# Optimization experiments

Measured on AMD Instinct MI355X. Metric: run time of the kernel, lower is better.

## Reference

```python
import jax, jax.numpy as jnp
import numpy as np

B, N, F = 2, 2048, 256
H = 8
O = F // H  # nhid = 32
L = 3       # stacked GraphAttentionLayers
ALPHA = 0.2
NEG = jnp.float32(-1e15)


def setup_inputs() -> dict:
    key = jax.random.key(0)
    ks = jax.random.split(key, 6)
    x = jax.random.normal(ks[0], (B, N, F), dtype=jnp.float32)
    adj = jax.random.randint(ks[1], (B, N, N), 0, 2, dtype=jnp.int32)
    # per-layer multi-head params: W [L,H,F,O], a [L,H,2O]
    W_heads = jax.random.normal(ks[2], (L, H, F, O), dtype=jnp.float32) * 0.1
    a_heads = jax.random.normal(ks[3], (L, H, 2 * O), dtype=jnp.float32) * 0.1
    # per-layer out_att params (single head, F->F)
    W_out = jax.random.normal(ks[4], (L, F, F), dtype=jnp.float32) * 0.05
    a_out = jax.random.normal(ks[5], (L, 2 * F), dtype=jnp.float32) * 0.05
    return {"x": x, "adj": adj, "W_heads": W_heads, "a_heads": a_heads,
            "W_out": W_out, "a_out": a_out}


def _gat_heads(h, mask, W, a1, a2):
    """h: [B,N,F], mask: [B,N,N] bool, W: [H,F,O], a1/a2: [H,O] -> [B,H,N,O]."""
    Wh = jnp.einsum('bnf,hfo->bhno', h, W)
    s1 = jnp.einsum('bhno,ho->bhn', Wh, a1)   # a[:O] projection
    s2 = jnp.einsum('bhno,ho->bhn', Wh, a2)   # a[O:] projection
    e = s1[:, :, :, None] + s2[:, :, None, :]  # additive score [B,H,N,N]
    e = jnp.where(e > 0, e, ALPHA * e)         # LeakyReLU(alpha)
    e = jnp.where(mask[:, None, :, :], e, NEG)
    att = jax.nn.softmax(e, axis=-1)           # dropout is identity in eval
    hp = jnp.einsum('bhnm,bhmo->bhno', att, Wh)
    return jax.nn.elu(hp)                      # activate_function inside head


def reference(x, adj, W_heads, a_heads, W_out, a_out):
    mask = adj > 0
    h = x
    for l in range(L):
        a1 = a_heads[l, :, :O]
        a2 = a_heads[l, :, O:]
        hh = _gat_heads(h, mask, W_heads[l], a1, a2)      # [B,H,N,O]
        h = jnp.transpose(hh, (0, 2, 1, 3)).reshape(B, N, F)  # concat heads
        ao1 = a_out[l, :F][None]
        ao2 = a_out[l, F:][None]
        ho = _gat_heads(h, mask, W_out[l][None], ao1, ao2)[:, 0]  # [B,N,F]
        h = jax.nn.elu(ho)  # extra F.elu in GraphAttentionLayer (elu twice)
    return h
```

## Files before the change

### kernel.cpp

```cpp
#include <hip/hip_runtime.h>
#include <math.h>

#if __has_builtin(__builtin_amdgcn_exp2f)
#define EXP2(x) __builtin_amdgcn_exp2f(x)
#else
#define EXP2(x) exp2f(x)
#endif

#define ALPHA_LRELU 0.2f
#define LOG2E 1.4426950408889634f
#define ESHIFT 6.0f
#define BIGM 1024.0f

constexpr int Bc = 2, Nn = 2048, Ff = 256, Hh = 8, Oo = 32;

typedef _Float16 f16;
typedef f16 f16x8 __attribute__((ext_vector_type(8)));
typedef f16 f16x4 __attribute__((ext_vector_type(4)));
typedef float f32x4 __attribute__((ext_vector_type(4)));
typedef unsigned long long u64;
typedef unsigned u32;

__global__ __launch_bounds__(256) void prep_kernel(
    const int* __restrict__ adj, const float* __restrict__ x,
    const float* __restrict__ W_heads, const float* __restrict__ W_out,
    u32* __restrict__ maskT, f16* __restrict__ Af, f16* __restrict__ WTF,
    float* __restrict__ sbuf) {
    const int B = blockIdx.x;
    const int t = threadIdx.x;
    int g = B * 256 + t;
    if (g < 221184) sbuf[g] = 0.f;

    if (B < 768) {
        for (int idx = g; idx < Bc * Nn * Nn; idx += 768 * 256) {
            u64 bl = __ballot(adj[idx] != 0);
            int lane = t & 63;
            int i = (idx >> 11) & 2047;
            int b = idx >> 22;
            int c32 = ((idx & 2047) & ~63) >> 5;
            if (lane == 0)
                maskT[((size_t)b * 64 + c32) * 2048 + i] = (u32)bl;
            else if (lane == 1)
                maskT[((size_t)b * 64 + c32 + 1) * 2048 + i] = (u32)(bl >> 32);
        }
    } else if (B < 896) {
        int w = t >> 6, lane = t & 63;
        int am = lane & 15, aq = lane >> 4;
#pragma unroll
        for (int it = 0; it < 4; ++it) {
            int slot = (B - 768) * 4 + w + it * 512;
            int mt = slot >> 3, c = slot & 7;
            const float* ap = x + ((size_t)mt * 16 + am) * Ff + c * 32 + aq * 8;
            f32x4 v0 = *(const f32x4*)ap;
            f32x4 v1 = *(const f32x4*)(ap + 4);
            f16x8 o;
#pragma unroll
            for (int i = 0; i < 4; ++i) { o[i] = (f16)v0[i]; o[4 + i] = (f16)v1[i]; }
            *(f16x8*)&Af[(size_t)slot * 512 + lane * 8] = o;
        }
    } else {
#pragma unroll
        for (int it = 0; it < 3; ++it) {
            int unit = (B - 896) * 3 + it;
            int y = unit >> 6, bx = unit & 63;
            int ll = y >> 1, st = y & 1;
            int col = bx * 4 + (t >> 6);
            int k0 = (t & 63) * 4;
            const float* src;
            int stride;
            if (st == 0) {
                src = W_heads + (((size_t)ll * Hh + (col >> 5)) * Ff) * Oo + (col & 31);
                stride = Oo;
            } else {
                src = W_out + (size_t)ll * Ff * Ff + col;
                stride = Ff;
            }
            f16x4 v;
#pragma unroll
            for (int i = 0; i < 4; ++i) v[i] = (f16)src[(size_t)(k0 + i) * stride];
            int cg = col >> 4, am = col & 15;
            int c = k0 >> 5, aq = (k0 >> 3) & 3, i0 = k0 & 7;
            *(f16x4*)&WTF[(((size_t)y * 16 + cg) * 8 + c) * 512 +
                          (aq * 16 + am) * 8 + i0] = v;
        }
    }
}

__global__ __launch_bounds__(256) void gemm_wave(
    const f16* __restrict__ Af, const f16* __restrict__ WTF,
    const float* __restrict__ pa, f16* __restrict__ WhFrag,
    float* __restrict__ s1, float* __restrict__ s2,
    int G, int Ofull, int oshift) {
    int t = threadIdx.x;
    int w = t >> 6, lane = t & 63;
    int am = lane & 15, aq = lane >> 4;
    int mt = blockIdx.x * 4 + w;
    int colb = blockIdx.y * 32;

    const f16* ap = Af + (size_t)(mt * 8) * 512 + lane * 8;
    const f16* bp0 = WTF + (size_t)((colb >> 4) * 8) * 512 + lane * 8;
    const f16* bp1 = bp0 + 8 * 512;

    f16x8 av[8], bv0[8], bv1[8];
#pragma unroll
    for (int c = 0; c < 8; ++c) {
        av[c] = *(const f16x8*)(ap + c * 512);
        bv0[c] = *(const f16x8*)(bp0 + c * 512);
        bv1[c] = *(const f16x8*)(bp1 + c * 512);
    }
    f32x4 acc0 = {0.f, 0.f, 0.f, 0.f}, acc1 = acc0;
#pragma unroll
    for (int c = 0; c < 8; ++c) {
        acc0 = __builtin_amdgcn_mfma_f32_16x16x32_f16(av[c], bv0[c], acc0, 0, 0, 0);
        acc1 = __builtin_amdgcn_mfma_f32_16x16x32_f16(av[c], bv1[c], acc1, 0, 0, 0);
    }

    int m0 = mt * 16;
    int b = m0 >> 11;
    int nn0 = (m0 & 2047) + aq * 4;
    int cO = (m0 & 2047) >> 5;
    int aq_p = ((mt & 1) << 1) | (aq >> 1);
    int i0p = (aq & 1) << 2;
    int g = colb >> oshift;
    size_t bg = (size_t)b * G + g;
    int cg = (colb & (Ofull - 1)) >> 4;

    f16x4 c40, c41;
#pragma unroll
    for (int e = 0; e < 4; ++e) { c40[e] = (f16)acc0[e]; c41[e] = (f16)acc1[e]; }
    *(f16x4*)&WhFrag[(((bg * (Ofull >> 4) + cg) * 64 + cO) * 512) +
                     (aq_p * 16 + am) * 8 + i0p] = c40;
    *(f16x4*)&WhFrag[(((bg * (Ofull >> 4) + cg + 1) * 64 + cO) * 512) +
                     (aq_p * 16 + am) * 8 + i0p] = c41;

    int o0 = (colb & (Ofull - 1)) + am;
    const float* a1p = pa + 2 * (size_t)g * Ofull;
    float a10 = a1p[o0], a11 = a1p[o0 + 16];
    float a20 = a1p[Ofull + o0], a21 = a1p[Ofull + o0 + 16];
#pragma unroll
    for (int e = 0; e < 4; ++e) {
        float p1 = acc0[e] * a10 + acc1[e] * a11;
        float p2 = acc0[e] * a20 + acc1[e] * a21;
#pragma unroll
        for (int s = 1; s < 16; s <<= 1) {
            p1 += __shfl_xor(p1, s);
            p2 += __shfl_xor(p2, s);
        }
        if (am == 0) {
            size_t sidx = bg * Nn + nn0 + e;
            atomicAdd(&s1[sidx], p1);
            atomicAdd(&s2[sidx], p2);
        }
    }
}

template <int CGW, int NW, bool OUT, bool FINAL>
__global__ __launch_bounds__(NW * 64) void attn_kernel(
    const f16* __restrict__ WhFrag, const float* __restrict__ s1,
    const float* __restrict__ s2, const u32* __restrict__ maskT,
    float* __restrict__ dst, f16* __restrict__ AfOut) {
    constexpr float C0 = -ESHIFT * LOG2E - BIGM;
    constexpr int NCG = OUT ? 16 : 2;
    constexpr int COLS = (NW / 4) * CGW * 16;
    constexpr int TSTR = COLS + 8;
    __shared__ float Ls[NW][2][64];
    __shared__ float As[NW][64][2 * CGW * 4];
    __shared__ f16 T[2][16 * TSTR];

    int t = threadIdx.x;
    int w = t >> 6, lane = t & 63;
    int am = lane & 15, aq = lane >> 4;
    int ch = w >> 2;
    int js = w & 3;
    int i0 = blockIdx.x * 32;
    int bz = blockIdx.z;
    int b = OUT ? bz : (bz >> 3);
    int cg0 = OUT ? blockIdx.y * ((NW / 4) * CGW) + ch * CGW : 0;
    int dstcol = OUT ? cg0 * 16 : (bz & 7) * Oo;

    const f16* bp[CGW];
#pragma unroll
    for (int i = 0; i < CGW; ++i)
        bp[i] = WhFrag + ((size_t)bz * NCG + cg0 + i) * 64 * 512 + lane * 8;
    const float* s2p = s2 + (size_t)bz * Nn + aq * 8;
    float s1v0 = s1[(size_t)bz * Nn + i0 + am];
    float s1v1 = s1[(size_t)bz * Nn + i0 + 16 + am];
    const u32* mtp0 = maskT + (size_t)b * 64 * 2048 + i0 + am;
    const u32* mtp1 = mtp0 + 16;

    f32x4 acc[2][CGW] = {};
    float lacc0 = 0.f, lacc1 = 0.f;

    int cbeg = js * 16, cend = cbeg + 16;

    f16x8 xb[CGW], yb[CGW];
    f32x4 xv0, xv1, yv0, yv1;
    u32 xm0, xm1, ym0, ym1;
    auto ld = [&](int c, f16x8 (&bb)[CGW], f32x4& v0, f32x4& v1,
                  u32& m0, u32& m1) {
#pragma unroll
        for (int i = 0; i < CGW; ++i) bb[i] = *(const f16x8*)(bp[i] + c * 512);
        v0 = *(const f32x4*)(s2p + c * 32);
        v1 = *(const f32x4*)(s2p + c * 32 + 4);
        m0 = mtp0[c * 2048];
        m1 = mtp1[c * 2048];
    };
    auto comp = [&](f16x8 (&bb)[CGW], f32x4 v0, f32x4 v1, u32 m0, u32 m1) {
        u32 bits0 = (m0 >> (aq * 8)) & 0xffu;
        u32 bits1 = (m1 >> (aq * 8)) & 0xffu;
        f16x8 af0, af1;
#pragma unroll
        for (int k = 0; k < 8; ++k) {
            float sv = (k < 4 ? v0[k] : v1[k - 4]);
            float x0 = s1v0 + sv;
            float x1 = s1v1 + sv;
            float lr0 = fmaxf(x0, ALPHA_LRELU * x0);
            float lr1 = fmaxf(x1, ALPHA_LRELU * x1);
            float bf0 = (float)((bits0 >> k) & 1u);
            float bf1 = (float)((bits1 >> k) & 1u);
            float p0 = EXP2(fmaf(bf0, BIGM, fmaf(lr0, LOG2E, C0)));
            float p1 = EXP2(fmaf(bf1, BIGM, fmaf(lr1, LOG2E, C0)));
            lacc0 += p0;
            lacc1 += p1;
            af0[k] = (f16)p0;
            af1[k] = (f16)p1;
        }
#pragma unroll
        for (int i = 0; i < CGW; ++i) {
            acc[0][i] = __builtin_amdgcn_mfma_f32_16x16x32_f16(af0, bb[i], acc[0][i], 0, 0, 0);
            acc[1][i] = __builtin_amdgcn_mfma_f32_16x16x32_f16(af1, bb[i], acc[1][i], 0, 0, 0);
        }
    };

    ld(cbeg, xb, xv0, xv1, xm0, xm1);
    ld(cbeg + 1, yb, yv0, yv1, ym0, ym1);
    for (int c = cbeg; c < cend; c += 2) {
        comp(xb, xv0, xv1, xm0, xm1);
        ld(c + 2 < cend ? c + 2 : cbeg, xb, xv0, xv1, xm0, xm1);
        comp(yb, yv0, yv1, ym0, ym1);
        ld(c + 3 < cend ? c + 3 : cbeg, yb, yv0, yv1, ym0, ym1);
    }

    lacc0 += __shfl_xor(lacc0, 16);
    lacc0 += __shfl_xor(lacc0, 32);
    lacc1 += __shfl_xor(lacc1, 16);
    lacc1 += __shfl_xor(lacc1, 32);

    Ls[w][0][lane] = lacc0;
    Ls[w][1][lane] = lacc1;
#pragma unroll
    for (int tt = 0; tt < 2; ++tt)
#pragma unroll
        for (int i = 0; i < CGW; ++i)
#pragma unroll
            for (int e = 0; e < 4; ++e)
                As[w][lane][tt * CGW * 4 + i * 4 + e] = acc[tt][i][e];
    __syncthreads();

    if ((w & 3) < 2) {
        int tt = w & 3;
        float lt = Ls[ch * 4 + 0][tt][lane] + Ls[ch * 4 + 1][tt][lane] +
                   Ls[ch * 4 + 2][tt][lane] + Ls[ch * 4 + 3][tt][lane];
        f16* Tw = T[tt];
#pragma unroll
        for (int i = 0; i < CGW; ++i) {
            f32x4 a;
#pragma unroll
            for (int e = 0; e < 4; ++e)
                a[e] = As[ch * 4 + 0][lane][tt * CGW * 4 + i * 4 + e] +
                       As[ch * 4 + 1][lane][tt * CGW * 4 + i * 4 + e] +
                       As[ch * 4 + 2][lane][tt * CGW * 4 + i * 4 + e] +
                       As[ch * 4 + 3][lane][tt * CGW * 4 + i * 4 + e];
#pragma unroll
            for (int e = 0; e < 4; ++e) {
                int r = aq * 4 + e;
                float li = __shfl(lt, r);
                float v = a[e] / li;
                v = v > 0.f ? v : __expf(v) - 1.f;
                if (OUT) v = v > 0.f ? v : __expf(v) - 1.f;
                if (FINAL) {
                    dst[((size_t)b * Nn + i0 + tt * 16 + r) * Ff + dstcol +
                        i * 16 + am] = v;
                } else {
                    Tw[r * TSTR + ch * CGW * 16 + i * 16 + am] = (f16)v;
                }
            }
        }
        if (!FINAL) {
            int mt = (b * Nn + i0 + tt * 16) >> 4;
#pragma unroll
            for (int s = 0; s < CGW / 2; ++s) {
                f16x8 o = *(const f16x8*)&Tw[am * TSTR + ch * CGW * 16 +
                                             s * 32 + aq * 8];
                int c = (dstcol >> 5) + s;
                *(f16x8*)&AfOut[(size_t)(mt * 8 + c) * 512 + lane * 8] = o;
            }
        }
    }
}

extern "C" void kernel_launch(void* const* d_in, const int* in_sizes, int n_in,
                              void* d_out, int out_size, void* d_ws, size_t ws_size,
                              hipStream_t stream) {
    const float* x = (const float*)d_in[0];
    const int* adj = (const int*)d_in[1];
    const float* W_heads = (const float*)d_in[2];
    const float* a_heads = (const float*)d_in[3];
    const float* W_out = (const float*)d_in[4];
    const float* a_out = (const float*)d_in[5];
    float* out = (float*)d_out;

    float* ws = (float*)d_ws;
    const size_t M = (size_t)Bc * Nn * Ff;
    f16* Af_a = (f16*)ws;
    f16* Af_b = (f16*)(ws + M / 2);
    f16* WhFrag = (f16*)(ws + M);
    u32* maskT = (u32*)(ws + 3 * M / 2);
    f16* WTF = (f16*)(ws + 3 * M / 2 + M / 4);
    float* sbuf = ws + 3 * M / 2 + M / 4 + 196608;
    const size_t SH = (size_t)Bc * Hh * Nn;
    const size_t SO = (size_t)Bc * Nn;
    const size_t SL = 2 * SH + 2 * SO;

    prep_kernel<<<1024, 256, 0, stream>>>(adj, x, W_heads, W_out,
                                          maskT, Af_a, WTF, sbuf);

    for (int l = 0; l < 3; ++l) {
        float* s1h = sbuf + l * SL;
        float* s2h = s1h + SH;
        float* s1o = s2h + SH;
        float* s2o = s1o + SO;

        gemm_wave<<<dim3((Bc * Nn) / 64, Ff / 32), 256, 0, stream>>>(
            Af_a, WTF + (size_t)(2 * l) * Ff * Ff,
            a_heads + (size_t)l * Hh * 2 * Oo, WhFrag, s1h, s2h, Hh, Oo, 5);
        attn_kernel<2, 4, false, false><<<dim3(Nn / 32, 1, Bc * Hh), 256, 0, stream>>>(
            WhFrag, s1h, s2h, maskT, nullptr, Af_b);

        gemm_wave<<<dim3((Bc * Nn) / 64, Ff / 32), 256, 0, stream>>>(
            Af_b, WTF + (size_t)(2 * l + 1) * Ff * Ff,
            a_out + (size_t)l * 2 * Ff, WhFrag, s1o, s2o, 1, Ff, 8);
        if (l == 2) {
            attn_kernel<4, 8, true, true><<<dim3(Nn / 32, Ff / 128, Bc), 512, 0, stream>>>(
                WhFrag, s1o, s2o, maskT, out, nullptr);
        } else {
            attn_kernel<4, 8, true, false><<<dim3(Nn / 32, Ff / 128, Bc), 512, 0, stream>>>(
                WhFrag, s1o, s2o, maskT, nullptr, Af_a);
        }
    }
}
```

Baseline: 265.3 us.

## Fuse all layers into a persistent megakernel with hierarchical grid barriers

Replaces the prep kernel and the 12 per-layer GEMM and attention launches with one persistent kernel of 512 blocks. The blocks step through the prep, GEMM and attention phases and meet at a two-level atomic grid barrier between phases. A small init kernel zeroes the score accumulators and the barrier counters. This removes per-launch overhead and the tail idle time at each kernel boundary. In exchange, the OUT attention phase now runs on 256-thread blocks instead of 512, and the barrier assumes all 512 blocks are resident at once, which hangs if they are not.

```diff
diff --git a/kernel.cpp b/kernel.cpp
--- a/kernel.cpp
+++ b/kernel.cpp
@@ -13,6 +13,7 @@
 #define BIGM 1024.0f
 
 constexpr int Bc = 2, Nn = 2048, Ff = 256, Hh = 8, Oo = 32;
+constexpr int NBLK = 512;
 
 typedef _Float16 f16;
 typedef f16 f16x8 __attribute__((ext_vector_type(8)));
@@ -21,18 +22,259 @@
 typedef unsigned long long u64;
 typedef unsigned u32;
 
-__global__ __launch_bounds__(256) void prep_kernel(
+__global__ __launch_bounds__(256) void init_kernel(float* __restrict__ sbuf,
+                                                   u32* __restrict__ bar) {
+    for (int g = blockIdx.x * 256 + threadIdx.x; g < 221184; g += NBLK * 256)
+        sbuf[g] = 0.f;
+    int g = blockIdx.x * 256 + threadIdx.x;
+    if (g < 544) bar[g] = 0;
+}
+
+__device__ __forceinline__ void gridbar(u32* bar, int ph) {
+    __syncthreads();
+    if (threadIdx.x == 0) {
+        __threadfence();
+        u32* lv1 = bar + 32 + (blockIdx.x & 15) * 32;
+        u32 old = __hip_atomic_fetch_add(lv1, 1u, __ATOMIC_RELAXED,
+                                         __HIP_MEMORY_SCOPE_AGENT);
+        if (old == (u32)(ph * 32 + 31))
+            __hip_atomic_fetch_add(bar, 1u, __ATOMIC_RELAXED,
+                                   __HIP_MEMORY_SCOPE_AGENT);
+        while (__hip_atomic_load(bar, __ATOMIC_RELAXED,
+                                 __HIP_MEMORY_SCOPE_AGENT) <
+               (u32)(ph * 16 + 16))
+            __builtin_amdgcn_s_sleep(2);
+        __threadfence();
+    }
+    __syncthreads();
+}
+
+__device__ __forceinline__ void gemm_phase(
+    const f16* __restrict__ Af, const f16* __restrict__ WTF,
+    const float* __restrict__ pa, f16* __restrict__ WhFrag,
+    float* __restrict__ s1, float* __restrict__ s2,
+    int G, int Ofull, int oshift, int xb, int yb) {
+    int t = threadIdx.x;
+    int w = t >> 6, lane = t & 63;
+    int am = lane & 15, aq = lane >> 4;
+    int mt = xb * 4 + w;
+    int colb = yb * 32;
+
+    const f16* ap = Af + (size_t)(mt * 8) * 512 + lane * 8;
+    const f16* bp0 = WTF + (size_t)((colb >> 4) * 8) * 512 + lane * 8;
+    const f16* bp1 = bp0 + 8 * 512;
+
+    f16x8 av[8], bv0[8], bv1[8];
+#pragma unroll
+    for (int c = 0; c < 8; ++c) {
+        av[c] = *(const f16x8*)(ap + c * 512);
+        bv0[c] = *(const f16x8*)(bp0 + c * 512);
+        bv1[c] = *(const f16x8*)(bp1 + c * 512);
+    }
+    f32x4 acc0 = {0.f, 0.f, 0.f, 0.f}, acc1 = acc0;
+#pragma unroll
+    for (int c = 0; c < 8; ++c) {
+        acc0 = __builtin_amdgcn_mfma_f32_16x16x32_f16(av[c], bv0[c], acc0, 0, 0, 0);
+        acc1 = __builtin_amdgcn_mfma_f32_16x16x32_f16(av[c], bv1[c], acc1, 0, 0, 0);
+    }
+
+    int m0 = mt * 16;
+    int b = m0 >> 11;
+    int nn0 = (m0 & 2047) + aq * 4;
+    int cO = (m0 & 2047) >> 5;
+    int aq_p = ((mt & 1) << 1) | (aq >> 1);
+    int i0p = (aq & 1) << 2;
+    int g = colb >> oshift;
+    size_t bg = (size_t)b * G + g;
+    int cg = (colb & (Ofull - 1)) >> 4;
+
+    f16x4 c40, c41;
+#pragma unroll
+    for (int e = 0; e < 4; ++e) { c40[e] = (f16)acc0[e]; c41[e] = (f16)acc1[e]; }
+    *(f16x4*)&WhFrag[(((bg * (Ofull >> 4) + cg) * 64 + cO) * 512) +
+                     (aq_p * 16 + am) * 8 + i0p] = c40;
+    *(f16x4*)&WhFrag[(((bg * (Ofull >> 4) + cg + 1) * 64 + cO) * 512) +
+                     (aq_p * 16 + am) * 8 + i0p] = c41;
+
+    int o0 = (colb & (Ofull - 1)) + am;
+    const float* a1p = pa + 2 * (size_t)g * Ofull;
+    float a10 = a1p[o0], a11 = a1p[o0 + 16];
+    float a20 = a1p[Ofull + o0], a21 = a1p[Ofull + o0 + 16];
+#pragma unroll
+    for (int e = 0; e < 4; ++e) {
+        float p1 = acc0[e] * a10 + acc1[e] * a11;
+        float p2 = acc0[e] * a20 + acc1[e] * a21;
+#pragma unroll
+        for (int s = 1; s < 16; s <<= 1) {
+            p1 += __shfl_xor(p1, s);
+            p2 += __shfl_xor(p2, s);
+        }
+        if (am == 0) {
+            size_t sidx = bg * Nn + nn0 + e;
+            atomicAdd(&s1[sidx], p1);
+            atomicAdd(&s2[sidx], p2);
+        }
+    }
+}
+
+template <int CGW, bool OUT, bool FINAL>
+__device__ __forceinline__ void attn_phase(
+    const f16* __restrict__ WhFrag, const float* __restrict__ s1,
+    const float* __restrict__ s2, const u32* __restrict__ maskT,
+    float* __restrict__ dst, f16* __restrict__ AfOut,
+    int xb, int yq, int bz,
+    float* __restrict__ LsS, float* __restrict__ AsS, f16* __restrict__ TS) {
+    constexpr float C0 = -ESHIFT * LOG2E - BIGM;
+    constexpr int NCG = OUT ? 16 : 2;
+    constexpr int TSTR = 72;
+
+    int t = threadIdx.x;
+    int w = t >> 6, lane = t & 63;
+    int am = lane & 15, aq = lane >> 4;
+    int i0 = xb * 32;
+    int b = OUT ? bz : (bz >> 3);
+    int cg0 = OUT ? yq * CGW : 0;
+    int dstcol = OUT ? cg0 * 16 : (bz & 7) * Oo;
+
+    const f16* bp[CGW];
+#pragma unroll
+    for (int i = 0; i < CGW; ++i)
+        bp[i] = WhFrag + ((size_t)bz * NCG + cg0 + i) * 64 * 512 + lane * 8;
+    const float* s2p = s2 + (size_t)bz * Nn + aq * 8;
+    float s1v0 = s1[(size_t)bz * Nn + i0 + am];
+    float s1v1 = s1[(size_t)bz * Nn + i0 + 16 + am];
+    const u32* mtp0 = maskT + (size_t)b * 64 * 2048 + i0 + am;
+    const u32* mtp1 = mtp0 + 16;
+
+    f32x4 acc[2][CGW] = {};
+    float lacc0 = 0.f, lacc1 = 0.f;
+
+    int cbeg = w * 16, cend = cbeg + 16;
+
+    f16x8 xb_[CGW], yb_[CGW];
+    f32x4 xv0, xv1, yv0, yv1;
+    u32 xm0, xm1, ym0, ym1;
+    auto ld = [&](int c, f16x8 (&bb)[CGW], f32x4& v0, f32x4& v1,
+                  u32& m0, u32& m1) {
+#pragma unroll
+        for (int i = 0; i < CGW; ++i) bb[i] = *(const f16x8*)(bp[i] + c * 512);
+        v0 = *(const f32x4*)(s2p + c * 32);
+        v1 = *(const f32x4*)(s2p + c * 32 + 4);
+        m0 = mtp0[c * 2048];
+        m1 = mtp1[c * 2048];
+    };
+    auto comp = [&](f16x8 (&bb)[CGW], f32x4 v0, f32x4 v1, u32 m0, u32 m1) {
+        u32 bits0 = (m0 >> (aq * 8)) & 0xffu;
+        u32 bits1 = (m1 >> (aq * 8)) & 0xffu;
+        f16x8 af0, af1;
+#pragma unroll
+        for (int k = 0; k < 8; ++k) {
+            float sv = (k < 4 ? v0[k] : v1[k - 4]);
+            float x0 = s1v0 + sv;
+            float x1 = s1v1 + sv;
+            float lr0 = fmaxf(x0, ALPHA_LRELU * x0);
+            float lr1 = fmaxf(x1, ALPHA_LRELU * x1);
+            float bf0 = (float)((bits0 >> k) & 1u);
+            float bf1 = (float)((bits1 >> k) & 1u);
+            float p0 = EXP2(fmaf(bf0, BIGM, fmaf(lr0, LOG2E, C0)));
+            float p1 = EXP2(fmaf(bf1, BIGM, fmaf(lr1, LOG2E, C0)));
+            lacc0 += p0;
+            lacc1 += p1;
+            af0[k] = (f16)p0;
+            af1[k] = (f16)p1;
+        }
+#pragma unroll
+        for (int i = 0; i < CGW; ++i) {
+            acc[0][i] = __builtin_amdgcn_mfma_f32_16x16x32_f16(af0, bb[i], acc[0][i], 0, 0, 0);
+            acc[1][i] = __builtin_amdgcn_mfma_f32_16x16x32_f16(af1, bb[i], acc[1][i], 0, 0, 0);
+        }
+    };
+
+    ld(cbeg, xb_, xv0, xv1, xm0, xm1);
+    ld(cbeg + 1, yb_, yv0, yv1, ym0, ym1);
+    for (int c = cbeg; c < cend; c += 2) {
+        comp(xb_, xv0, xv1, xm0, xm1);
+        ld(c + 2 < cend ? c + 2 : cbeg, xb_, xv0, xv1, xm0, xm1);
+        comp(yb_, yv0, yv1, ym0, ym1);
+        ld(c + 3 < cend ? c + 3 : cbeg, yb_, yv0, yv1, ym0, ym1);
+    }
+
+    lacc0 += __shfl_xor(lacc0, 16);
+    lacc0 += __shfl_xor(lacc0, 32);
+    lacc1 += __shfl_xor(lacc1, 16);
+    lacc1 += __shfl_xor(lacc1, 32);
+
+    LsS[(w * 2 + 0) * 64 + lane] = lacc0;
+    LsS[(w * 2 + 1) * 64 + lane] = lacc1;
+#pragma unroll
+    for (int tt = 0; tt < 2; ++tt)
+#pragma unroll
+        for (int i = 0; i < CGW; ++i)
+#pragma unroll
+            for (int e = 0; e < 4; ++e)
+                AsS[(w * 64 + lane) * 32 + tt * CGW * 4 + i * 4 + e] =
+                    acc[tt][i][e];
+    __syncthreads();
+
+    if (w < 2) {
+        int tt = w;
+        float lt = LsS[(0 * 2 + tt) * 64 + lane] + LsS[(1 * 2 + tt) * 64 + lane] +
+                   LsS[(2 * 2 + tt) * 64 + lane] + LsS[(3 * 2 + tt) * 64 + lane];
+        f16* Tw = &TS[tt * 16 * TSTR];
+#pragma unroll
+        for (int i = 0; i < CGW; ++i) {
+            f32x4 a;
+#pragma unroll
+            for (int e = 0; e < 4; ++e)
+                a[e] = AsS[(0 * 64 + lane) * 32 + tt * CGW * 4 + i * 4 + e] +
+                       AsS[(1 * 64 + lane) * 32 + tt * CGW * 4 + i * 4 + e] +
+                       AsS[(2 * 64 + lane) * 32 + tt * CGW * 4 + i * 4 + e] +
+                       AsS[(3 * 64 + lane) * 32 + tt * CGW * 4 + i * 4 + e];
+#pragma unroll
+            for (int e = 0; e < 4; ++e) {
+                int r = aq * 4 + e;
+                float li = __shfl(lt, r);
+                float v = a[e] / li;
+                v = v > 0.f ? v : __expf(v) - 1.f;
+                if (OUT) v = v > 0.f ? v : __expf(v) - 1.f;
+                if (FINAL) {
+                    dst[((size_t)b * Nn + i0 + tt * 16 + r) * Ff + dstcol +
+                        i * 16 + am] = v;
+                } else {
+                    Tw[r * TSTR + i * 16 + am] = (f16)v;
+                }
+            }
+        }
+        if (!FINAL) {
+            int mt = (b * Nn + i0 + tt * 16) >> 4;
+#pragma unroll
+            for (int s = 0; s < CGW / 2; ++s) {
+                f16x8 o = *(const f16x8*)&Tw[am * TSTR + s * 32 + aq * 8];
+                int c = (dstcol >> 5) + s;
+                *(f16x8*)&AfOut[(size_t)(mt * 8 + c) * 512 + lane * 8] = o;
+            }
+        }
+    }
+    __syncthreads();
+}
+
+__global__ __launch_bounds__(256, 2) void mega_kernel(
     const int* __restrict__ adj, const float* __restrict__ x,
-    const float* __restrict__ W_heads, const float* __restrict__ W_out,
-    u32* __restrict__ maskT, f16* __restrict__ Af, f16* __restrict__ WTF,
-    float* __restrict__ sbuf) {
+    const float* __restrict__ W_heads, const float* __restrict__ a_heads,
+    const float* __restrict__ W_out, const float* __restrict__ a_out,
+    float* __restrict__ out, f16* __restrict__ Af_a, f16* __restrict__ Af_b,
+    f16* __restrict__ WhFrag, u32* __restrict__ maskT, f16* __restrict__ WTF,
+    float* __restrict__ sbuf, u32* __restrict__ bar) {
+    __shared__ float LsS[4 * 2 * 64];
+    __shared__ float AsS[4 * 64 * 32];
+    __shared__ f16 TS[2 * 16 * 72];
+
     const int B = blockIdx.x;
     const int t = threadIdx.x;
-    int g = B * 256 + t;
-    if (g < 221184) sbuf[g] = 0.f;
-
-    if (B < 768) {
-        for (int idx = g; idx < Bc * Nn * Nn; idx += 768 * 256) {
+    int ph = 0;
+
+    if (B < 384) {
+        for (int idx = B * 256 + t; idx < Bc * Nn * Nn; idx += 384 * 256) {
             u64 bl = __ballot(adj[idx] != 0);
             int lane = t & 63;
             int i = (idx >> 11) & 2047;
@@ -43,12 +285,12 @@
             else if (lane == 1)
                 maskT[((size_t)b * 64 + c32 + 1) * 2048 + i] = (u32)(bl >> 32);
         }
-    } else if (B < 896) {
+    } else if (B < 448) {
         int w = t >> 6, lane = t & 63;
         int am = lane & 15, aq = lane >> 4;
 #pragma unroll
-        for (int it = 0; it < 4; ++it) {
-            int slot = (B - 768) * 4 + w + it * 512;
+        for (int it = 0; it < 8; ++it) {
+            int slot = (B - 384) * 4 + w + it * 256;
             int mt = slot >> 3, c = slot & 7;
             const float* ap = x + ((size_t)mt * 16 + am) * Ff + c * 32 + aq * 8;
             f32x4 v0 = *(const f32x4*)ap;
@@ -56,12 +298,12 @@
             f16x8 o;
 #pragma unroll
             for (int i = 0; i < 4; ++i) { o[i] = (f16)v0[i]; o[4 + i] = (f16)v1[i]; }
-            *(f16x8*)&Af[(size_t)slot * 512 + lane * 8] = o;
+            *(f16x8*)&Af_a[(size_t)slot * 512 + lane * 8] = o;
         }
     } else {
 #pragma unroll
-        for (int it = 0; it < 3; ++it) {
-            int unit = (B - 896) * 3 + it;
+        for (int it = 0; it < 6; ++it) {
+            int unit = (B - 448) * 6 + it;
             int y = unit >> 6, bx = unit & 63;
             int ll = y >> 1, st = y & 1;
             int col = bx * 4 + (t >> 6);
@@ -84,217 +326,38 @@
                           (aq * 16 + am) * 8 + i0] = v;
         }
     }
-}
-
-__global__ __launch_bounds__(256) void gemm_wave(
-    const f16* __restrict__ Af, const f16* __restrict__ WTF,
-    const float* __restrict__ pa, f16* __restrict__ WhFrag,
-    float* __restrict__ s1, float* __restrict__ s2,
-    int G, int Ofull, int oshift) {
-    int t = threadIdx.x;
-    int w = t >> 6, lane = t & 63;
-    int am = lane & 15, aq = lane >> 4;
-    int mt = blockIdx.x * 4 + w;
-    int colb = blockIdx.y * 32;
-
-    const f16* ap = Af + (size_t)(mt * 8) * 512 + lane * 8;
-    const f16* bp0 = WTF + (size_t)((colb >> 4) * 8) * 512 + lane * 8;
-    const f16* bp1 = bp0 + 8 * 512;
-
-    f16x8 av[8], bv0[8], bv1[8];
-#pragma unroll
-    for (int c = 0; c < 8; ++c) {
-        av[c] = *(const f16x8*)(ap + c * 512);
-        bv0[c] = *(const f16x8*)(bp0 + c * 512);
-        bv1[c] = *(const f16x8*)(bp1 + c * 512);
-    }
-    f32x4 acc0 = {0.f, 0.f, 0.f, 0.f}, acc1 = acc0;
-#pragma unroll
-    for (int c = 0; c < 8; ++c) {
-        acc0 = __builtin_amdgcn_mfma_f32_16x16x32_f16(av[c], bv0[c], acc0, 0, 0, 0);
-        acc1 = __builtin_amdgcn_mfma_f32_16x16x32_f16(av[c], bv1[c], acc1, 0, 0, 0);
-    }
-
-    int m0 = mt * 16;
-    int b = m0 >> 11;
-    int nn0 = (m0 & 2047) + aq * 4;
-    int cO = (m0 & 2047) >> 5;
-    int aq_p = ((mt & 1) << 1) | (aq >> 1);
-    int i0p = (aq & 1) << 2;
-    int g = colb >> oshift;
-    size_t bg = (size_t)b * G + g;
-    int cg = (colb & (Ofull - 1)) >> 4;
-
-    f16x4 c40, c41;
-#pragma unroll
-    for (int e = 0; e < 4; ++e) { c40[e] = (f16)acc0[e]; c41[e] = (f16)acc1[e]; }
-    *(f16x4*)&WhFrag[(((bg * (Ofull >> 4) + cg) * 64 + cO) * 512) +
-                     (aq_p * 16 + am) * 8 + i0p] = c40;
-    *(f16x4*)&WhFrag[(((bg * (Ofull >> 4) + cg + 1) * 64 + cO) * 512) +
-                     (aq_p * 16 + am) * 8 + i0p] = c41;
-
-    int o0 = (colb & (Ofull - 1)) + am;
-    const float* a1p = pa + 2 * (size_t)g * Ofull;
-    float a10 = a1p[o0], a11 = a1p[o0 + 16];
-    float a20 = a1p[Ofull + o0], a21 = a1p[Ofull + o0 + 16];
-#pragma unroll
-    for (int e = 0; e < 4; ++e) {
-        float p1 = acc0[e] * a10 + acc1[e] * a11;
-        float p2 = acc0[e] * a20 + acc1[e] * a21;
-#pragma unroll
-        for (int s = 1; s < 16; s <<= 1) {
-            p1 += __shfl_xor(p1, s);
-            p2 += __shfl_xor(p2, s);
-        }
-        if (am == 0) {
-            size_t sidx = bg * Nn + nn0 + e;
-            atomicAdd(&s1[sidx], p1);
-            atomicAdd(&s2[sidx], p2);
-        }
-    }
-}
-
-template <int CGW, int NW, bool OUT, bool FINAL>
-__global__ __launch_bounds__(NW * 64) void attn_kernel(
-    const f16* __restrict__ WhFrag, const float* __restrict__ s1,
-    const float* __restrict__ s2, const u32* __restrict__ maskT,
-    float* __restrict__ dst, f16* __restrict__ AfOut) {
-    constexpr float C0 = -ESHIFT * LOG2E - BIGM;
-    constexpr int NCG = OUT ? 16 : 2;
-    constexpr int COLS = (NW / 4) * CGW * 16;
-    constexpr int TSTR = COLS + 8;
-    __shared__ float Ls[NW][2][64];
-    __shared__ float As[NW][64][2 * CGW * 4];
-    __shared__ f16 T[2][16 * TSTR];
-
-    int t = threadIdx.x;
-    int w = t >> 6, lane = t & 63;
-    int am = lane & 15, aq = lane >> 4;
-    int ch = w >> 2;
-    int js = w & 3;
-    int i0 = blockIdx.x * 32;
-    int bz = blockIdx.z;
-    int b = OUT ? bz : (bz >> 3);
-    int cg0 = OUT ? blockIdx.y * ((NW / 4) * CGW) + ch * CGW : 0;
-    int dstcol = OUT ? cg0 * 16 : (bz & 7) * Oo;
-
-    const f16* bp[CGW];
-#pragma unroll
-    for (int i = 0; i < CGW; ++i)
-        bp[i] = WhFrag + ((size_t)bz * NCG + cg0 + i) * 64 * 512 + lane * 8;
-    const float* s2p = s2 + (size_t)bz * Nn + aq * 8;
-    float s1v0 = s1[(size_t)bz * Nn + i0 + am];
-    float s1v1 = s1[(size_t)bz * Nn + i0 + 16 + am];
-    const u32* mtp0 = maskT + (size_t)b * 64 * 2048 + i0 + am;
-    const u32* mtp1 = mtp0 + 16;
-
-    f32x4 acc[2][CGW] = {};
-    float lacc0 = 0.f, lacc1 = 0.f;
-
-    int cbeg = js * 16, cend = cbeg + 16;
-
-    f16x8 xb[CGW], yb[CGW];
-    f32x4 xv0, xv1, yv0, yv1;
-    u32 xm0, xm1, ym0, ym1;
-    auto ld = [&](int c, f16x8 (&bb)[CGW], f32x4& v0, f32x4& v1,
-                  u32& m0, u32& m1) {
-#pragma unroll
-        for (int i = 0; i < CGW; ++i) bb[i] = *(const f16x8*)(bp[i] + c * 512);
-        v0 = *(const f32x4*)(s2p + c * 32);
-        v1 = *(const f32x4*)(s2p + c * 32 + 4);
-        m0 = mtp0[c * 2048];
-        m1 = mtp1[c * 2048];
-    };
-    auto comp = [&](f16x8 (&bb)[CGW], f32x4 v0, f32x4 v1, u32 m0, u32 m1) {
-        u32 bits0 = (m0 >> (aq * 8)) & 0xffu;
-        u32 bits1 = (m1 >> (aq * 8)) & 0xffu;
-        f16x8 af0, af1;
-#pragma unroll
-        for (int k = 0; k < 8; ++k) {
-            float sv = (k < 4 ? v0[k] : v1[k - 4]);
-            float x0 = s1v0 + sv;
-            float x1 = s1v1 + sv;
-            float lr0 = fmaxf(x0, ALPHA_LRELU * x0);
-            float lr1 = fmaxf(x1, ALPHA_LRELU * x1);
-            float bf0 = (float)((bits0 >> k) & 1u);
-            float bf1 = (float)((bits1 >> k) & 1u);
-            float p0 = EXP2(fmaf(bf0, BIGM, fmaf(lr0, LOG2E, C0)));
-            float p1 = EXP2(fmaf(bf1, BIGM, fmaf(lr1, LOG2E, C0)));
-            lacc0 += p0;
-            lacc1 += p1;
-            af0[k] = (f16)p0;
-            af1[k] = (f16)p1;
-        }
-#pragma unroll
-        for (int i = 0; i < CGW; ++i) {
-            acc[0][i] = __builtin_amdgcn_mfma_f32_16x16x32_f16(af0, bb[i], acc[0][i], 0, 0, 0);
-            acc[1][i] = __builtin_amdgcn_mfma_f32_16x16x32_f16(af1, bb[i], acc[1][i], 0, 0, 0);
-        }
-    };
-
-    ld(cbeg, xb, xv0, xv1, xm0, xm1);
-    ld(cbeg + 1, yb, yv0, yv1, ym0, ym1);
-    for (int c = cbeg; c < cend; c += 2) {
-        comp(xb, xv0, xv1, xm0, xm1);
-        ld(c + 2 < cend ? c + 2 : cbeg, xb, xv0, xv1, xm0, xm1);
-        comp(yb, yv0, yv1, ym0, ym1);
-        ld(c + 3 < cend ? c + 3 : cbeg, yb, yv0, yv1, ym0, ym1);
-    }
-
-    lacc0 += __shfl_xor(lacc0, 16);
-    lacc0 += __shfl_xor(lacc0, 32);
-    lacc1 += __shfl_xor(lacc1, 16);
-    lacc1 += __shfl_xor(lacc1, 32);
-
-    Ls[w][0][lane] = lacc0;
-    Ls[w][1][lane] = lacc1;
-#pragma unroll
-    for (int tt = 0; tt < 2; ++tt)
-#pragma unroll
-        for (int i = 0; i < CGW; ++i)
-#pragma unroll
-            for (int e = 0; e < 4; ++e)
-                As[w][lane][tt * CGW * 4 + i * 4 + e] = acc[tt][i][e];
-    __syncthreads();
-
-    if ((w & 3) < 2) {
-        int tt = w & 3;
-        float lt = Ls[ch * 4 + 0][tt][lane] + Ls[ch * 4 + 1][tt][lane] +
-                   Ls[ch * 4 + 2][tt][lane] + Ls[ch * 4 + 3][tt][lane];
-        f16* Tw = T[tt];
-#pragma unroll
-        for (int i = 0; i < CGW; ++i) {
-            f32x4 a;
-#pragma unroll
-            for (int e = 0; e < 4; ++e)
-                a[e] = As[ch * 4 + 0][lane][tt * CGW * 4 + i * 4 + e] +
-                       As[ch * 4 + 1][lane][tt * CGW * 4 + i * 4 + e] +
-                       As[ch * 4 + 2][lane][tt * CGW * 4 + i * 4 + e] +
-                       As[ch * 4 + 3][lane][tt * CGW * 4 + i * 4 + e];
-#pragma unroll
-            for (int e = 0; e < 4; ++e) {
-                int r = aq * 4 + e;
-                float li = __shfl(lt, r);
-                float v = a[e] / li;
-                v = v > 0.f ? v : __expf(v) - 1.f;
-                if (OUT) v = v > 0.f ? v : __expf(v) - 1.f;
-                if (FINAL) {
-                    dst[((size_t)b * Nn + i0 + tt * 16 + r) * Ff + dstcol +
-                        i * 16 + am] = v;
-                } else {
-                    Tw[r * TSTR + ch * CGW * 16 + i * 16 + am] = (f16)v;
-                }
-            }
-        }
-        if (!FINAL) {
-            int mt = (b * Nn + i0 + tt * 16) >> 4;
-#pragma unroll
-            for (int s = 0; s < CGW / 2; ++s) {
-                f16x8 o = *(const f16x8*)&Tw[am * TSTR + ch * CGW * 16 +
-                                             s * 32 + aq * 8];
-                int c = (dstcol >> 5) + s;
-                *(f16x8*)&AfOut[(size_t)(mt * 8 + c) * 512 + lane * 8] = o;
-            }
+    gridbar(bar, ph++);
+
+    const size_t SH = (size_t)Bc * Hh * Nn;
+    const size_t SO = (size_t)Bc * Nn;
+    const size_t SL = 2 * SH + 2 * SO;
+
+    for (int l = 0; l < 3; ++l) {
+        float* s1h = sbuf + l * SL;
+        float* s2h = s1h + SH;
+        float* s1o = s2h + SH;
+        float* s2o = s1o + SO;
+
+        gemm_phase(Af_a, WTF + (size_t)(2 * l) * Ff * Ff,
+                   a_heads + (size_t)l * Hh * 2 * Oo, WhFrag, s1h, s2h,
+                   Hh, Oo, 5, B & 63, B >> 6);
+        gridbar(bar, ph++);
+        for (int u = B; u < 1024; u += NBLK)
+            attn_phase<2, false, false>(WhFrag, s1h, s2h, maskT, nullptr, Af_b,
+                                        u & 63, 0, u >> 6, LsS, AsS, TS);
+        gridbar(bar, ph++);
+
+        gemm_phase(Af_b, WTF + (size_t)(2 * l + 1) * Ff * Ff,
+                   a_out + (size_t)l * 2 * Ff, WhFrag, s1o, s2o,
+                   1, Ff, 8, B & 63, B >> 6);
+        gridbar(bar, ph++);
+        if (l == 2) {
+            attn_phase<4, true, true>(WhFrag, s1o, s2o, maskT, out, nullptr,
+                                      B & 63, (B >> 6) & 3, B >> 8, LsS, AsS, TS);
+        } else {
+            attn_phase<4, true, false>(WhFrag, s1o, s2o, maskT, nullptr, Af_a,
+                                       B & 63, (B >> 6) & 3, B >> 8, LsS, AsS, TS);
+            gridbar(bar, ph++);
         }
     }
 }
@@ -318,34 +381,10 @@
     u32* maskT = (u32*)(ws + 3 * M / 2);
     f16* WTF = (f16*)(ws + 3 * M / 2 + M / 4);
     float* sbuf = ws + 3 * M / 2 + M / 4 + 196608;
-    const size_t SH = (size_t)Bc * Hh * Nn;
-    const size_t SO = (size_t)Bc * Nn;
-    const size_t SL = 2 * SH + 2 * SO;
-
-    prep_kernel<<<1024, 256, 0, stream>>>(adj, x, W_heads, W_out,
-                                          maskT, Af_a, WTF, sbuf);
-
-    for (int l = 0; l < 3; ++l) {
-        float* s1h = sbuf + l * SL;
-        float* s2h = s1h + SH;
-        float* s1o = s2h + SH;
-        float* s2o = s1o + SO;
-
-        gemm_wave<<<dim3((Bc * Nn) / 64, Ff / 32), 256, 0, stream>>>(
-            Af_a, WTF + (size_t)(2 * l) * Ff * Ff,
-            a_heads + (size_t)l * Hh * 2 * Oo, WhFrag, s1h, s2h, Hh, Oo, 5);
-        attn_kernel<2, 4, false, false><<<dim3(Nn / 32, 1, Bc * Hh), 256, 0, stream>>>(
-            WhFrag, s1h, s2h, maskT, nullptr, Af_b);
-
-        gemm_wave<<<dim3((Bc * Nn) / 64, Ff / 32), 256, 0, stream>>>(
-            Af_b, WTF + (size_t)(2 * l + 1) * Ff * Ff,
-            a_out + (size_t)l * 2 * Ff, WhFrag, s1o, s2o, 1, Ff, 8);
-        if (l == 2) {
-            attn_kernel<4, 8, true, true><<<dim3(Nn / 32, Ff / 128, Bc), 512, 0, stream>>>(
-                WhFrag, s1o, s2o, maskT, out, nullptr);
-        } else {
-            attn_kernel<4, 8, true, false><<<dim3(Nn / 32, Ff / 128, Bc), 512, 0, stream>>>(
-                WhFrag, s1o, s2o, maskT, nullptr, Af_a);
-        }
-    }
-}
+    u32* bar = (u32*)(sbuf + 221184);
+
+    init_kernel<<<NBLK, 256, 0, stream>>>(sbuf, bar);
+    mega_kernel<<<NBLK, 256, 0, stream>>>(
+        adj, x, W_heads, a_heads, W_out, a_out, out,
+        Af_a, Af_b, WhFrag, maskT, WTF, sbuf, bar);
+}
```

Result: slower. 530.3 us (+99.9%).
